# Kernel optimization log

Measured on AMD Instinct MI355X. Metric: run time of the kernel, lower is better.

The kernel has to match this reference:

```python
import jax, jax.numpy as jnp
import numpy as np

B, T, F = 256, 2048, 20
H_NODES = 256


def _heaviside(x):
    # smooth heaviside approx used throughout the original module
    return (jnp.tanh(10.0 * x) + 1.0) * 0.5


def _evap(wu, wl, wd, pet):
    h = _heaviside
    et1 = h(wu - pet) * pet + h(pet - wu) * wu
    rp = h(pet - et1) * (pet - et1)  # h(-(pet-et1))*0 term vanishes
    et22 = h(rp - wl) * wl + h(wl - rp) * rp
    et2 = h(rp) * et22
    et33 = h(rp - et2 - wd) * wd + h(wd - (rp - et2)) * (rp - et2)
    et3 = h(rp - et2) * et33
    return et1, et2, et3


def _runoff(wu, wl, wd, p, wum, wlm, wdm, b, c):
    wum = wum * 19.9 + 0.1
    wlm = wlm * 30.0 + 60.0
    wdm = wdm * 60.0 + 60.0
    c = c * 0.19 + 0.01
    b = b * 0.3 + 0.1
    w_total = wum + wlm + wdm
    s = c * (wu / w_total) ** 2 + b * (wl / w_total) ** 2
    return _heaviside(p - s) * (p - s)


def _partition(runoff, k1, k2, k3):
    k1 = k1 * 0.69 + 0.01
    k2 = k2 * 0.69 + 0.01
    k3 = k3 * 0.89 + 0.01
    sr = k1 * runoff
    itf = k2 * (runoff - sr)
    bf = k3 * (runoff - sr - itf)
    return sr, itf, bf


def setup_inputs() -> dict:
    key = jax.random.key(0)
    ks = jax.random.split(key, 7)
    u = lambda k, shp: jax.random.uniform(k, shp, jnp.float32, -0.05, 0.05)
    inputs = jax.random.uniform(ks[0], (B, T, F), jnp.float32)
    return {
        "inputs": inputs,
        "w1": u(ks[1], (15, H_NODES)),
        "b1": jnp.zeros((H_NODES,), jnp.float32),
        "w2": u(ks[2], (H_NODES, 64)),
        "b2": jnp.zeros((64,), jnp.float32),
        "w3": u(ks[3], (64, 8)),
        "b3": jnp.zeros((8,), jnp.float32),
    }


def reference(inputs, w1, b1, w2, b2, w3, b3):
    pet = inputs[..., 0:1]
    tmean = inputs[..., 1:2]
    p = inputs[..., 2:3]
    attrs = inputs[..., 5:]  # [B,T,15]

    # static-attribute -> physical-parameter MLP
    h1 = jnp.tanh(attrs @ w1 + b1)
    h2 = jnp.tanh(h1 @ w2 + b2)
    params = jax.nn.sigmoid(h2 @ w3 + b3)  # [B,T,8]

    xs = jnp.concatenate([pet, p, tmean, params], axis=-1)  # [B,T,11]

    def step(state, x):
        wu, wl, wd = state[:, 0:1], state[:, 1:2], state[:, 2:3]
        pet_t, p_t = x[:, 0:1], x[:, 1:2]
        et1, et2, et3 = _evap(wu, wl, wd, pet_t)
        clip = lambda d: jnp.clip(d, -1e5, 1e5)
        wu_n = wu + clip(p_t - et1)
        wl_n = wl + clip(p_t - et1 - et2)
        wd_n = wd + clip(p_t - et1 - et2 - et3)
        ns = jnp.concatenate([wu_n, wl_n, wd_n], axis=1)  # [B,3]
        return ns, ns

    init = jnp.zeros((inputs.shape[0], 3), inputs.dtype)
    _, outs = jax.lax.scan(step, init, jnp.swapaxes(xs, 0, 1))  # [T,B,3]
    outputs = jnp.swapaxes(outs, 0, 1)  # [B,T,3]

    wu, wl, wd = outputs[..., 0:1], outputs[..., 1:2], outputs[..., 2:3]
    wum, wlm, wdm = params[..., 0:1], params[..., 1:2], params[..., 2:3]
    b, c = params[..., 3:4], params[..., 4:5]
    k1, k2, k3 = params[..., 5:6], params[..., 6:7], params[..., 7:8]

    et1, et2, et3 = _evap(wu, wl, wd, pet)
    # NOTE: original call() swaps (wl,wd) and (wlm,wdm) here - kept faithful
    runoff = _runoff(wu, wd, wl, p, wum, wdm, wlm, b, c)
    sr, itf, bf = _partition(runoff, k1, k2, k3)
    total_q = sr + itf * 0.5 + bf * 0.25  # flow routing
    return total_q  # [B,T,1]
```

## Files before the change

kernel.cpp:

```cpp
#include <hip/hip_runtime.h>

#define B_ 256
#define T_ 2048
#define F_ 20
#define NT (B_*T_)
#define CH 16
#define NCH (T_/CH)

typedef __bf16 bf16x8 __attribute__((ext_vector_type(8)));
typedef float  f32x4  __attribute__((ext_vector_type(4)));

__device__ __forceinline__ float ex2(float x){ return __builtin_amdgcn_exp2f(x); }
__device__ __forceinline__ float rcpf_(float x){ return __builtin_amdgcn_rcpf(x); }

#define K10F 28.853900817779268f
#define INVK 0.034657359027997264f
#define K1F   2.8853900817779268f
#define LOG2E 1.4426950408889634f

__device__ __forceinline__ float hside(float x){ return 1.0f - rcpf_(ex2(K10F*x) + 1.0f); }
__device__ __forceinline__ float tanh_f(float z){ return 1.0f - 2.0f*rcpf_(ex2(K1F*z) + 1.0f); }
__device__ __forceinline__ float sigmoid_f(float z){ return rcpf_(1.0f + ex2(-LOG2E*z)); }


__global__ __launch_bounds__(512, 4) void fused_kernel(const float* __restrict__ in,
    const float* __restrict__ w1, const float* __restrict__ b1,
    const float* __restrict__ w2, const float* __restrict__ b2,
    const float* __restrict__ w3, const float* __restrict__ b3,
    float* __restrict__ ws){
  extern __shared__ char sm[];
  float* params2 = ws + 2*(size_t)NT;

  if (blockIdx.x < 8) {
    float2* wwT = (float2*)ws;
    float2* ppL = (float2*)sm;
    float2* dkb = (float2*)(sm + 8192);
    float2* rhb = (float2*)(sm + 24576);
    float2* qbb = (float2*)(sm + 32768);
    float*  wub = (float*)(sm + 40960);
    float*  wdb = (float*)(sm + 57344);

    int tid  = threadIdx.x;
    int wv   = tid >> 6;
    int l64  = tid & 63;
    bool act = l64 < 32;
    int lane = l64 & 31;
    int boff = blockIdx.x * 32;
    int bmy  = boff + lane;

    float Wu = 0.0f, WL = 0.0f, WD = 0.0f;

    if (wv == 4 && act){
    float2 v[CH];
      #pragma unroll
      for (int s = 0; s < CH; ++s){
        float4 r4 = *(const float4*)(in + ((size_t)bmy*T_ + s)*F_);
        v[s] = make_float2(r4.x, r4.z);
      }
      #pragma unroll
      for (int s = 0; s < CH; ++s)
        ppL[s*32 + lane] = make_float2(K10F*v[s].x, K10F*(v[s].y - v[s].x));
    }
    __syncthreads();

    for (int it = 0; it < NCH + 4; ++it){
      if (wv == 0){
        int c = it;
        if (c < NCH && act){
          int par = c & 1, pd = c & 3, pw = c & 7;
          float2 pe[CH];
          #pragma unroll
          for (int s = 0; s < CH; ++s) pe[s] = ppL[(par*CH + s)*32 + lane];
          #pragma unroll
          for (int s = 0; s < CH; ++s){
            float t1 = Wu - pe[s].x;
            float r  = rcpf_(ex2(t1) + 1.0f);
            float dK = -t1*r;
            float BASE = pe[s].y + dK;
            float Wn = Wu + BASE;
            dkb[(pd*CH + s)*32 + lane] = make_float2(dK, BASE);
            wub[(pw*CH + s)*32 + lane] = Wn;
            Wu = Wn;
          }
        }
      } else if (wv == 1){
        int c = it - 1;
        if (c >= 0 && c < NCH && act){
          int par = c & 1, pd = c & 3;
          float dk[CH];
          #pragma unroll
          for (int s = 0; s < CH; ++s) dk[s] = dkb[(pd*CH + s)*32 + lane].x;
          #pragma unroll
          for (int s = 0; s < CH; ++s){
            float r1  = rcpf_(ex2(dk[s]) + 1.0f);
            float RP  = fmaf(-dk[s], r1, dk[s]);
            float HRP = 1.0f - rcpf_(ex2(RP) + 1.0f);
            rhb[(par*CH + s)*32 + lane] = make_float2(RP, HRP);
          }
        }
      } else if (wv == 2){
        int c = it - 2;
        if (c >= 0 && c < NCH && act){
          int par = c & 1, pd = c & 3;
          float2 rh[CH]; float bs[CH];
          #pragma unroll
          for (int s = 0; s < CH; ++s) rh[s] = rhb[(par*CH + s)*32 + lane];
          #pragma unroll
          for (int s = 0; s < CH; ++s) bs[s] = dkb[(pd*CH + s)*32 + lane].y;
          #pragma unroll
          for (int s = 0; s < CH; ++s){
            float D2   = rh[s].x - WL;
            float r    = rcpf_(ex2(D2) + 1.0f);
            float et22 = fmaf(D2, r, WL);
            float WLB  = WL + bs[s];
            float Wn   = fmaf(-rh[s].y, et22, WLB);
            float ET2  = rh[s].y * et22;
            qbb[(par*CH + s)*32 + lane] = make_float2(rh[s].x - ET2, bs[s] - ET2);
            WL = Wn;
          }
        }
      } else if (wv == 3){
        int c = it - 3;
        if (c >= 0 && c < NCH && act){
          int par = c & 1;
          float2 qb[CH];
          #pragma unroll
          for (int s = 0; s < CH; ++s) qb[s] = qbb[(par*CH + s)*32 + lane];
          #pragma unroll
          for (int s = 0; s < CH; ++s){
            float hqv  = 1.0f - rcpf_(ex2(qb[s].x) + 1.0f);
            float D3   = qb[s].x - WD;
            float r    = rcpf_(ex2(D3) + 1.0f);
            float et33 = fmaf(D3, r, WD);
            float WDB  = WD + qb[s].y;
            float Wn   = fmaf(-hqv, et33, WDB);
            wdb[(par*CH + s)*32 + lane] = Wn;
            WD = Wn;
          }
        }
      } else if (wv == 4){
        int cn = it + 1;
        if (cn < NCH && act){
          float2 v[CH];
          #pragma unroll
          for (int s = 0; s < CH; ++s){
            float4 r4 = *(const float4*)(in + ((size_t)bmy*T_ + cn*CH + s)*F_);
            v[s] = make_float2(r4.x, r4.z);
          }
          int par = cn & 1;
          #pragma unroll
          for (int s = 0; s < CH; ++s)
            ppL[(par*CH + s)*32 + lane] = make_float2(K10F*v[s].x, K10F*(v[s].y - v[s].x));
        }
      } else if (wv == 5){
        int c = it - 4;
        if (c >= 0 && c < NCH && act){
          int pw = c & 7, par = c & 1;
          float wuv[CH], wdv[CH];
          #pragma unroll
          for (int s = 0; s < CH; ++s) wuv[s] = wub[(pw*CH + s)*32 + lane];
          #pragma unroll
          for (int s = 0; s < CH; ++s) wdv[s] = wdb[(par*CH + s)*32 + lane];
          float2* dst = &wwT[(size_t)bmy*T_ + c*CH];
          #pragma unroll
          for (int s = 0; s < CH; ++s)
            dst[s] = make_float2(wuv[s]*INVK, wdv[s]*INVK);
        }
      }
      __syncthreads();
    }
    return;
  }

  __bf16* w1f  = (__bf16*)sm;
  __bf16* w2f  = (__bf16*)(sm + 8192);
  float*  b1s  = (float*)(sm + 40960);
  float*  b2s  = (float*)(sm + 41984);
  float*  w3s  = (float*)(sm + 42240);
  float*  b3s  = (float*)(sm + 44288);
  __bf16* hbufA= (__bf16*)(sm + 44320);

  int tid = threadIdx.x;

  for (int s = tid; s < 16*32*8; s += 512) w1f[s] = (__bf16)0.0f;
  __syncthreads();
  for (int idx = tid; idx < 15*256; idx += 512){
    int k = idx >> 8, n = idx & 255;
    int ct = n >> 4;
    int l  = ((k>>3)*16) + (n & 15);
    int j  = k & 7;
    w1f[(ct*32 + l)*8 + j] = (__bf16)w1[idx];
  }
  for (int idx = tid; idx < 256*64; idx += 512){
    int k = idx >> 6, n = idx & 63;
    int kb = k >> 5;
    int lq = (k >> 3) & 3;
    int j  = k & 7;
    int ct = n >> 4;
    int l  = lq*16 + (n & 15);
    w2f[((kb*4 + ct)*64 + l)*8 + j] = (__bf16)w2[idx];
  }
  if (tid < 256) b1s[tid] = b1[tid];
  if (tid < 64)  b2s[tid] = b2[tid];
  if (tid < 512) w3s[tid] = w3[tid];
  if (tid < 8)   b3s[tid] = b3[tid];
  __syncthreads();

  int lane = tid & 63;
  int wv   = tid >> 6;
  int m    = lane & 15;
  int q    = lane >> 4;
  int r0   = (blockIdx.x - 8)*128 + wv*16;

  int rho = r0 + m;
  const float* ap = in + (size_t)rho*F_ + 5;
  bf16x8 a1;
  #pragma unroll
  for (int j = 0; j < 8; ++j){
    int k = q*8 + j;
    float v = (k < 15) ? ap[k] : 0.0f;
    a1[j] = (__bf16)v;
  }

  __bf16* hb = hbufA + wv*1152;
  f32x4 zero4 = {0.0f, 0.0f, 0.0f, 0.0f};
  bf16x8 zero8;
  #pragma unroll
  for (int j = 0; j < 8; ++j) zero8[j] = (__bf16)0.0f;

  f32x4 acc2[4] = {zero4, zero4, zero4, zero4};

  #pragma unroll
  for (int p = 0; p < 4; ++p){
    #pragma unroll
    for (int c4 = 0; c4 < 4; ++c4){
      int ct = p*4 + c4;
      bf16x8 bw = zero8;
      if (lane < 32) bw = *(const bf16x8*)&w1f[(ct*32 + lane)*8];
      f32x4 c1 = __builtin_amdgcn_mfma_f32_16x16x32_bf16(a1, bw, zero4, 0, 0, 0);
      int f = c4*16 + m;
      float bb = b1s[p*64 + f];
      #pragma unroll
      for (int i = 0; i < 4; ++i){
        float h = tanh_f(c1[i] + bb);
        hb[(q*4 + i)*72 + f] = (__bf16)h;
      }
    }
    #pragma unroll
    for (int kb = 0; kb < 2; ++kb){
      bf16x8 a2 = *(const bf16x8*)&hb[m*72 + q*8 + kb*32];
      #pragma unroll
      for (int ct = 0; ct < 4; ++ct){
        bf16x8 bw2 = *(const bf16x8*)&w2f[(((p*2 + kb)*4 + ct)*64 + lane)*8];
        acc2[ct] = __builtin_amdgcn_mfma_f32_16x16x32_bf16(a2, bw2, acc2[ct], 0, 0, 0);
      }
    }
  }

  #pragma unroll
  for (int ct = 0; ct < 4; ++ct){
    int f = ct*16 + m;
    float bb = b2s[f];
    #pragma unroll
    for (int i = 0; i < 4; ++i){
      float h = tanh_f(acc2[ct][i] + bb);
      hb[(q*4 + i)*72 + f] = (__bf16)h;
    }
  }

  float z0 = b3s[2*q], z1 = b3s[2*q + 1];
  #pragma unroll
  for (int kb3 = 0; kb3 < 8; ++kb3){
    bf16x8 hv8 = *(const bf16x8*)&hb[m*72 + kb3*8];
    #pragma unroll
    for (int j = 0; j < 8; ++j){
      float hv = (float)hv8[j];
      int k = kb3*8 + j;
      z0 = fmaf(hv, w3s[k*8 + 2*q],     z0);
      z1 = fmaf(hv, w3s[k*8 + 2*q + 1], z1);
    }
  }
  float2 outp = make_float2(sigmoid_f(z0), sigmoid_f(z1));
  *(float2*)&params2[(size_t)rho*8 + 2*q] = outp;
}

__global__ __launch_bounds__(256) void final_kernel(const float* __restrict__ in,
                                                    const float* __restrict__ ws,
                                                    float* __restrict__ out){
  int rho = blockIdx.x*256 + threadIdx.x;
  if (rho >= NT) return;
  const float2* wwT = (const float2*)ws;
  const float* params2 = ws + 2*(size_t)NT;

  float p  = in[(size_t)rho*F_ + 2];
  float2 w = wwT[rho];
  float wu = w.x, wd = w.y;
  const float4* pp = (const float4*)(params2 + (size_t)rho*8);
  float4 p0 = pp[0], p1 = pp[1];
  float wum   = fmaf(p0.x, 19.9f, 0.1f);
  float wlm_s = fmaf(p0.z, 30.0f, 60.0f);
  float wdm_s = fmaf(p0.y, 60.0f, 60.0f);
  float cc = fmaf(p1.x, 0.19f, 0.01f);
  float bcoef = fmaf(p0.w, 0.30f, 0.10f);
  float wt = wum + wlm_s + wdm_s;
  float xu = wu / wt;
  float xd = wd / wt;
  float s  = cc*xu*xu + bcoef*xd*xd;
  float ps = p - s;
  float runoff = hside(ps)*ps;
  float k1p = fmaf(p1.y, 0.69f, 0.01f);
  float k2p = fmaf(p1.z, 0.69f, 0.01f);
  float k3p = fmaf(p1.w, 0.89f, 0.01f);
  float sr  = k1p*runoff;
  float itf = k2p*(runoff - sr);
  float bf  = k3p*(runoff - sr - itf);
  out[rho] = sr + 0.5f*itf + 0.25f*bf;
}

extern "C" void kernel_launch(void* const* d_in, const int* in_sizes, int n_in,
                              void* d_out, int out_size, void* d_ws, size_t ws_size,
                              hipStream_t stream) {
  const float* in = (const float*)d_in[0];
  const float* w1 = (const float*)d_in[1];
  const float* b1 = (const float*)d_in[2];
  const float* w2 = (const float*)d_in[3];
  const float* b2 = (const float*)d_in[4];
  const float* w3 = (const float*)d_in[5];
  const float* b3 = (const float*)d_in[6];
  float* out = (float*)d_out;
  float* ws  = (float*)d_ws;

  fused_kernel<<<NT/128 + 8,  512, 62752, stream>>>(in, w1, b1, w2, b2, w3, b3, ws);
  final_kernel<<<NT/256,      256, 0,     stream>>>(in, ws, out);
}
```

Measured before the change: 245.0 us.

## Deepen scan wavefront pipeline to nine stages and stage precipitation for final kernel

Splits the serial scan pipeline into more warp-specialized stages, moving the heaviside computations for RP and qv off the recurrence-critical waves. Dedicated writer waves store wu and wd as separate contiguous float4 arrays. The loader wave double-buffers global input in registers and also writes a compact precipitation array, so the final kernel no longer does strided reads of the input. Blocks grow to 576 threads with static shared memory, which adds pipeline latency, raises register pressure and changes occupancy for the MLP blocks, where the extra wave idles.

```diff
diff --git a/kernel.cpp b/kernel.cpp
--- a/kernel.cpp
+++ b/kernel.cpp
@@ -23,148 +23,229 @@
 __device__ __forceinline__ float sigmoid_f(float z){ return rcpf_(1.0f + ex2(-LOG2E*z)); }
 
 
-__global__ __launch_bounds__(512, 4) void fused_kernel(const float* __restrict__ in,
+struct ScanS {
+  float2 ppL[2][CH][32];
+  float  dkR[2][CH][32];
+  float  bsR[4][CH][32];
+  float  wuR[2][CH][32];
+  float  rpR[4][CH][32];
+  float  hrR[2][CH][32];
+  float  qvR[4][CH][32];
+  float  b2R[4][CH][32];
+  float  hqR[2][CH][32];
+  float  wdR[2][CH][32];
+};
+struct MlpS {
+  __bf16 w1f[16*32*8];
+  __bf16 w2f[32*64*8];
+  float  b1s[256];
+  float  b2s[64];
+  float  w3s[512];
+  float  b3s[8];
+  __bf16 hbuf[8][1152];
+};
+union SMu { ScanS s; MlpS m; };
+
+__global__ __launch_bounds__(576) void fused_kernel(const float* __restrict__ in,
     const float* __restrict__ w1, const float* __restrict__ b1,
     const float* __restrict__ w2, const float* __restrict__ b2,
     const float* __restrict__ w3, const float* __restrict__ b3,
     float* __restrict__ ws){
-  extern __shared__ char sm[];
+  __shared__ SMu smu;
   float* params2 = ws + 2*(size_t)NT;
 
   if (blockIdx.x < 8) {
-    float2* wwT = (float2*)ws;
-    float2* ppL = (float2*)sm;
-    float2* dkb = (float2*)(sm + 8192);
-    float2* rhb = (float2*)(sm + 24576);
-    float2* qbb = (float2*)(sm + 32768);
-    float*  wub = (float*)(sm + 40960);
-    float*  wdb = (float*)(sm + 57344);
-
+    ScanS& S = smu.s;
+    float* wuT = ws;
+    float* wdT = ws + (size_t)NT;
+    float* pT  = ws + 10*(size_t)NT;
     int tid  = threadIdx.x;
     int wv   = tid >> 6;
-    int l64  = tid & 63;
-    bool act = l64 < 32;
-    int lane = l64 & 31;
-    int boff = blockIdx.x * 32;
-    int bmy  = boff + lane;
+    int lane = tid & 31;
+    bool act = (tid & 63) < 32;
+    int bmy  = blockIdx.x*32 + lane;
+    const float* inb = in + (size_t)bmy*T_*F_;
 
     float Wu = 0.0f, WL = 0.0f, WD = 0.0f;
-
-    if (wv == 4 && act){
     float2 v[CH];
+
+    if (wv == 6 && act){
       #pragma unroll
       for (int s = 0; s < CH; ++s){
-        float4 r4 = *(const float4*)(in + ((size_t)bmy*T_ + s)*F_);
+        float4 r4 = *(const float4*)(inb + (size_t)s*F_);
         v[s] = make_float2(r4.x, r4.z);
       }
       #pragma unroll
       for (int s = 0; s < CH; ++s)
-        ppL[s*32 + lane] = make_float2(K10F*v[s].x, K10F*(v[s].y - v[s].x));
+        S.ppL[0][s][lane] = make_float2(K10F*v[s].x, K10F*(v[s].y - v[s].x));
+      float* pdst = &pT[(size_t)bmy*T_];
+      #pragma unroll
+      for (int g = 0; g < 4; ++g)
+        *(float4*)(pdst + g*4) = make_float4(v[g*4].y, v[g*4+1].y, v[g*4+2].y, v[g*4+3].y);
+      #pragma unroll
+      for (int s = 0; s < CH; ++s){
+        float4 r4 = *(const float4*)(inb + (size_t)(CH + s)*F_);
+        v[s] = make_float2(r4.x, r4.z);
+      }
     }
     __syncthreads();
 
-    for (int it = 0; it < NCH + 4; ++it){
+    for (int it = 0; it < NCH + 6; ++it){
       if (wv == 0){
         int c = it;
         if (c < NCH && act){
-          int par = c & 1, pd = c & 3, pw = c & 7;
           float2 pe[CH];
           #pragma unroll
-          for (int s = 0; s < CH; ++s) pe[s] = ppL[(par*CH + s)*32 + lane];
+          for (int s = 0; s < CH; ++s) pe[s] = S.ppL[c&1][s][lane];
+          float dk_[CH], bs_[CH], wu_[CH];
           #pragma unroll
           for (int s = 0; s < CH; ++s){
             float t1 = Wu - pe[s].x;
             float r  = rcpf_(ex2(t1) + 1.0f);
             float dK = -t1*r;
-            float BASE = pe[s].y + dK;
-            float Wn = Wu + BASE;
-            dkb[(pd*CH + s)*32 + lane] = make_float2(dK, BASE);
-            wub[(pw*CH + s)*32 + lane] = Wn;
-            Wu = Wn;
+            float BS = pe[s].y + dK;
+            Wu += BS;
+            dk_[s] = dK; bs_[s] = BS; wu_[s] = Wu;
           }
+          #pragma unroll
+          for (int s = 0; s < CH; ++s) S.dkR[c&1][s][lane] = dk_[s];
+          #pragma unroll
+          for (int s = 0; s < CH; ++s) S.bsR[c&3][s][lane] = bs_[s];
+          #pragma unroll
+          for (int s = 0; s < CH; ++s) S.wuR[c&1][s][lane] = wu_[s];
         }
       } else if (wv == 1){
         int c = it - 1;
         if (c >= 0 && c < NCH && act){
-          int par = c & 1, pd = c & 3;
-          float dk[CH];
-          #pragma unroll
-          for (int s = 0; s < CH; ++s) dk[s] = dkb[(pd*CH + s)*32 + lane].x;
+          float dk_[CH];
+          #pragma unroll
+          for (int s = 0; s < CH; ++s) dk_[s] = S.dkR[c&1][s][lane];
+          float rp_[CH];
           #pragma unroll
           for (int s = 0; s < CH; ++s){
-            float r1  = rcpf_(ex2(dk[s]) + 1.0f);
-            float RP  = fmaf(-dk[s], r1, dk[s]);
-            float HRP = 1.0f - rcpf_(ex2(RP) + 1.0f);
-            rhb[(par*CH + s)*32 + lane] = make_float2(RP, HRP);
+            float r1 = rcpf_(ex2(dk_[s]) + 1.0f);
+            rp_[s] = fmaf(-dk_[s], r1, dk_[s]);
           }
+          #pragma unroll
+          for (int s = 0; s < CH; ++s) S.rpR[c&3][s][lane] = rp_[s];
         }
       } else if (wv == 2){
         int c = it - 2;
         if (c >= 0 && c < NCH && act){
-          int par = c & 1, pd = c & 3;
-          float2 rh[CH]; float bs[CH];
-          #pragma unroll
-          for (int s = 0; s < CH; ++s) rh[s] = rhb[(par*CH + s)*32 + lane];
-          #pragma unroll
-          for (int s = 0; s < CH; ++s) bs[s] = dkb[(pd*CH + s)*32 + lane].y;
+          float rp_[CH];
+          #pragma unroll
+          for (int s = 0; s < CH; ++s) rp_[s] = S.rpR[c&3][s][lane];
+          float hr_[CH];
+          #pragma unroll
+          for (int s = 0; s < CH; ++s) hr_[s] = 1.0f - rcpf_(ex2(rp_[s]) + 1.0f);
+          #pragma unroll
+          for (int s = 0; s < CH; ++s) S.hrR[c&1][s][lane] = hr_[s];
+        }
+      } else if (wv == 3){
+        int c = it - 3;
+        if (c >= 0 && c < NCH && act){
+          float rp_[CH], hr_[CH], bs_[CH];
+          #pragma unroll
+          for (int s = 0; s < CH; ++s) rp_[s] = S.rpR[c&3][s][lane];
+          #pragma unroll
+          for (int s = 0; s < CH; ++s) hr_[s] = S.hrR[c&1][s][lane];
+          #pragma unroll
+          for (int s = 0; s < CH; ++s) bs_[s] = S.bsR[c&3][s][lane];
+          float qv_[CH], b2_[CH];
           #pragma unroll
           for (int s = 0; s < CH; ++s){
-            float D2   = rh[s].x - WL;
+            float D2   = rp_[s] - WL;
             float r    = rcpf_(ex2(D2) + 1.0f);
             float et22 = fmaf(D2, r, WL);
-            float WLB  = WL + bs[s];
-            float Wn   = fmaf(-rh[s].y, et22, WLB);
-            float ET2  = rh[s].y * et22;
-            qbb[(par*CH + s)*32 + lane] = make_float2(rh[s].x - ET2, bs[s] - ET2);
-            WL = Wn;
+            float WLB  = WL + bs_[s];
+            float ET2  = hr_[s]*et22;
+            WL = fmaf(-hr_[s], et22, WLB);
+            qv_[s] = rp_[s] - ET2;
+            b2_[s] = bs_[s] - ET2;
           }
-        }
-      } else if (wv == 3){
-        int c = it - 3;
-        if (c >= 0 && c < NCH && act){
-          int par = c & 1;
-          float2 qb[CH];
-          #pragma unroll
-          for (int s = 0; s < CH; ++s) qb[s] = qbb[(par*CH + s)*32 + lane];
+          #pragma unroll
+          for (int s = 0; s < CH; ++s) S.qvR[c&3][s][lane] = qv_[s];
+          #pragma unroll
+          for (int s = 0; s < CH; ++s) S.b2R[c&3][s][lane] = b2_[s];
+        }
+      } else if (wv == 4){
+        int c = it - 4;
+        if (c >= 0 && c < NCH && act){
+          float qv_[CH];
+          #pragma unroll
+          for (int s = 0; s < CH; ++s) qv_[s] = S.qvR[c&3][s][lane];
+          float hq_[CH];
+          #pragma unroll
+          for (int s = 0; s < CH; ++s) hq_[s] = 1.0f - rcpf_(ex2(qv_[s]) + 1.0f);
+          #pragma unroll
+          for (int s = 0; s < CH; ++s) S.hqR[c&1][s][lane] = hq_[s];
+        }
+      } else if (wv == 5){
+        int c = it - 5;
+        if (c >= 0 && c < NCH && act){
+          float qv_[CH], hq_[CH], b2_[CH];
+          #pragma unroll
+          for (int s = 0; s < CH; ++s) qv_[s] = S.qvR[c&3][s][lane];
+          #pragma unroll
+          for (int s = 0; s < CH; ++s) hq_[s] = S.hqR[c&1][s][lane];
+          #pragma unroll
+          for (int s = 0; s < CH; ++s) b2_[s] = S.b2R[c&3][s][lane];
+          float wd_[CH];
           #pragma unroll
           for (int s = 0; s < CH; ++s){
-            float hqv  = 1.0f - rcpf_(ex2(qb[s].x) + 1.0f);
-            float D3   = qb[s].x - WD;
+            float D3   = qv_[s] - WD;
             float r    = rcpf_(ex2(D3) + 1.0f);
             float et33 = fmaf(D3, r, WD);
-            float WDB  = WD + qb[s].y;
-            float Wn   = fmaf(-hqv, et33, WDB);
-            wdb[(par*CH + s)*32 + lane] = Wn;
-            WD = Wn;
+            float WDB  = WD + b2_[s];
+            WD = fmaf(-hq_[s], et33, WDB);
+            wd_[s] = WD;
           }
-        }
-      } else if (wv == 4){
-        int cn = it + 1;
-        if (cn < NCH && act){
-          float2 v[CH];
-          #pragma unroll
-          for (int s = 0; s < CH; ++s){
-            float4 r4 = *(const float4*)(in + ((size_t)bmy*T_ + cn*CH + s)*F_);
-            v[s] = make_float2(r4.x, r4.z);
+          #pragma unroll
+          for (int s = 0; s < CH; ++s) S.wdR[c&1][s][lane] = wd_[s];
+        }
+      } else if (wv == 6){
+        int n = it + 1;
+        if (n < NCH && act){
+          float2 w[CH];
+          #pragma unroll
+          for (int s = 0; s < CH; ++s) w[s] = v[s];
+          #pragma unroll
+          for (int s = 0; s < CH; ++s)
+            S.ppL[n&1][s][lane] = make_float2(K10F*w[s].x, K10F*(w[s].y - w[s].x));
+          float* pdst = &pT[(size_t)bmy*T_ + n*CH];
+          #pragma unroll
+          for (int g = 0; g < 4; ++g)
+            *(float4*)(pdst + g*4) = make_float4(w[g*4].y, w[g*4+1].y, w[g*4+2].y, w[g*4+3].y);
+          int n2 = it + 2;
+          if (n2 < NCH){
+            #pragma unroll
+            for (int s = 0; s < CH; ++s){
+              float4 r4 = *(const float4*)(inb + (size_t)(n2*CH + s)*F_);
+              v[s] = make_float2(r4.x, r4.z);
+            }
           }
-          int par = cn & 1;
-          #pragma unroll
-          for (int s = 0; s < CH; ++s)
-            ppL[(par*CH + s)*32 + lane] = make_float2(K10F*v[s].x, K10F*(v[s].y - v[s].x));
-        }
-      } else if (wv == 5){
-        int c = it - 4;
-        if (c >= 0 && c < NCH && act){
-          int pw = c & 7, par = c & 1;
-          float wuv[CH], wdv[CH];
-          #pragma unroll
-          for (int s = 0; s < CH; ++s) wuv[s] = wub[(pw*CH + s)*32 + lane];
-          #pragma unroll
-          for (int s = 0; s < CH; ++s) wdv[s] = wdb[(par*CH + s)*32 + lane];
-          float2* dst = &wwT[(size_t)bmy*T_ + c*CH];
-          #pragma unroll
-          for (int s = 0; s < CH; ++s)
-            dst[s] = make_float2(wuv[s]*INVK, wdv[s]*INVK);
+        }
+      } else if (wv == 7){
+        int c = it - 1;
+        if (c >= 0 && c < NCH && act){
+          float wu_[CH];
+          #pragma unroll
+          for (int s = 0; s < CH; ++s) wu_[s] = S.wuR[c&1][s][lane] * INVK;
+          float* dst = &wuT[(size_t)bmy*T_ + c*CH];
+          #pragma unroll
+          for (int g = 0; g < 4; ++g)
+            *(float4*)(dst + g*4) = make_float4(wu_[g*4], wu_[g*4+1], wu_[g*4+2], wu_[g*4+3]);
+        }
+      } else {
+        int c = it - 6;
+        if (c >= 0 && c < NCH && act){
+          float wd_[CH];
+          #pragma unroll
+          for (int s = 0; s < CH; ++s) wd_[s] = S.wdR[c&1][s][lane] * INVK;
+          float* dst = &wdT[(size_t)bmy*T_ + c*CH];
+          #pragma unroll
+          for (int g = 0; g < 4; ++g)
+            *(float4*)(dst + g*4) = make_float4(wd_[g*4], wd_[g*4+1], wd_[g*4+2], wd_[g*4+3]);
         }
       }
       __syncthreads();
@@ -172,42 +253,36 @@
     return;
   }
 
-  __bf16* w1f  = (__bf16*)sm;
-  __bf16* w2f  = (__bf16*)(sm + 8192);
-  float*  b1s  = (float*)(sm + 40960);
-  float*  b2s  = (float*)(sm + 41984);
-  float*  w3s  = (float*)(sm + 42240);
-  float*  b3s  = (float*)(sm + 44288);
-  __bf16* hbufA= (__bf16*)(sm + 44320);
-
+  MlpS& M = smu.m;
   int tid = threadIdx.x;
 
-  for (int s = tid; s < 16*32*8; s += 512) w1f[s] = (__bf16)0.0f;
+  for (int s = tid; s < 16*32*8; s += 576) M.w1f[s] = (__bf16)0.0f;
   __syncthreads();
-  for (int idx = tid; idx < 15*256; idx += 512){
+  for (int idx = tid; idx < 15*256; idx += 576){
     int k = idx >> 8, n = idx & 255;
     int ct = n >> 4;
     int l  = ((k>>3)*16) + (n & 15);
     int j  = k & 7;
-    w1f[(ct*32 + l)*8 + j] = (__bf16)w1[idx];
-  }
-  for (int idx = tid; idx < 256*64; idx += 512){
+    M.w1f[(ct*32 + l)*8 + j] = (__bf16)w1[idx];
+  }
+  for (int idx = tid; idx < 256*64; idx += 576){
     int k = idx >> 6, n = idx & 63;
     int kb = k >> 5;
     int lq = (k >> 3) & 3;
     int j  = k & 7;
     int ct = n >> 4;
     int l  = lq*16 + (n & 15);
-    w2f[((kb*4 + ct)*64 + l)*8 + j] = (__bf16)w2[idx];
-  }
-  if (tid < 256) b1s[tid] = b1[tid];
-  if (tid < 64)  b2s[tid] = b2[tid];
-  if (tid < 512) w3s[tid] = w3[tid];
-  if (tid < 8)   b3s[tid] = b3[tid];
+    M.w2f[((kb*4 + ct)*64 + l)*8 + j] = (__bf16)w2[idx];
+  }
+  if (tid < 256) M.b1s[tid] = b1[tid];
+  if (tid < 64)  M.b2s[tid] = b2[tid];
+  if (tid < 512) M.w3s[tid] = w3[tid];
+  if (tid < 8)   M.b3s[tid] = b3[tid];
   __syncthreads();
 
+  int wv = tid >> 6;
+  if (wv >= 8) return;
   int lane = tid & 63;
-  int wv   = tid >> 6;
   int m    = lane & 15;
   int q    = lane >> 4;
   int r0   = (blockIdx.x - 8)*128 + wv*16;
@@ -218,11 +293,11 @@
   #pragma unroll
   for (int j = 0; j < 8; ++j){
     int k = q*8 + j;
-    float v = (k < 15) ? ap[k] : 0.0f;
-    a1[j] = (__bf16)v;
-  }
-
-  __bf16* hb = hbufA + wv*1152;
+    float vv = (k < 15) ? ap[k] : 0.0f;
+    a1[j] = (__bf16)vv;
+  }
+
+  __bf16* hb = M.hbuf[wv];
   f32x4 zero4 = {0.0f, 0.0f, 0.0f, 0.0f};
   bf16x8 zero8;
   #pragma unroll
@@ -236,10 +311,10 @@
     for (int c4 = 0; c4 < 4; ++c4){
       int ct = p*4 + c4;
       bf16x8 bw = zero8;
-      if (lane < 32) bw = *(const bf16x8*)&w1f[(ct*32 + lane)*8];
+      if (lane < 32) bw = *(const bf16x8*)&M.w1f[(ct*32 + lane)*8];
       f32x4 c1 = __builtin_amdgcn_mfma_f32_16x16x32_bf16(a1, bw, zero4, 0, 0, 0);
       int f = c4*16 + m;
-      float bb = b1s[p*64 + f];
+      float bb = M.b1s[p*64 + f];
       #pragma unroll
       for (int i = 0; i < 4; ++i){
         float h = tanh_f(c1[i] + bb);
@@ -251,7 +326,7 @@
       bf16x8 a2 = *(const bf16x8*)&hb[m*72 + q*8 + kb*32];
       #pragma unroll
       for (int ct = 0; ct < 4; ++ct){
-        bf16x8 bw2 = *(const bf16x8*)&w2f[(((p*2 + kb)*4 + ct)*64 + lane)*8];
+        bf16x8 bw2 = *(const bf16x8*)&M.w2f[(((p*2 + kb)*4 + ct)*64 + lane)*8];
         acc2[ct] = __builtin_amdgcn_mfma_f32_16x16x32_bf16(a2, bw2, acc2[ct], 0, 0, 0);
       }
     }
@@ -260,7 +335,7 @@
   #pragma unroll
   for (int ct = 0; ct < 4; ++ct){
     int f = ct*16 + m;
-    float bb = b2s[f];
+    float bb = M.b2s[f];
     #pragma unroll
     for (int i = 0; i < 4; ++i){
       float h = tanh_f(acc2[ct][i] + bb);
@@ -268,7 +343,7 @@
     }
   }
 
-  float z0 = b3s[2*q], z1 = b3s[2*q + 1];
+  float z0 = M.b3s[2*q], z1 = M.b3s[2*q + 1];
   #pragma unroll
   for (int kb3 = 0; kb3 < 8; ++kb3){
     bf16x8 hv8 = *(const bf16x8*)&hb[m*72 + kb3*8];
@@ -276,25 +351,25 @@
     for (int j = 0; j < 8; ++j){
       float hv = (float)hv8[j];
       int k = kb3*8 + j;
-      z0 = fmaf(hv, w3s[k*8 + 2*q],     z0);
-      z1 = fmaf(hv, w3s[k*8 + 2*q + 1], z1);
+      z0 = fmaf(hv, M.w3s[k*8 + 2*q],     z0);
+      z1 = fmaf(hv, M.w3s[k*8 + 2*q + 1], z1);
     }
   }
   float2 outp = make_float2(sigmoid_f(z0), sigmoid_f(z1));
   *(float2*)&params2[(size_t)rho*8 + 2*q] = outp;
 }
 
-__global__ __launch_bounds__(256) void final_kernel(const float* __restrict__ in,
-                                                    const float* __restrict__ ws,
+__global__ __launch_bounds__(256) void final_kernel(const float* __restrict__ ws,
                                                     float* __restrict__ out){
   int rho = blockIdx.x*256 + threadIdx.x;
   if (rho >= NT) return;
-  const float2* wwT = (const float2*)ws;
+  const float* wuT = ws;
+  const float* wdT = ws + (size_t)NT;
   const float* params2 = ws + 2*(size_t)NT;
-
-  float p  = in[(size_t)rho*F_ + 2];
-  float2 w = wwT[rho];
-  float wu = w.x, wd = w.y;
+  const float* pT  = ws + 10*(size_t)NT;
+
+  float p  = pT[rho];
+  float wu = wuT[rho], wd = wdT[rho];
   const float4* pp = (const float4*)(params2 + (size_t)rho*8);
   float4 p0 = pp[0], p1 = pp[1];
   float wum   = fmaf(p0.x, 19.9f, 0.1f);
@@ -330,6 +405,6 @@
   float* out = (float*)d_out;
   float* ws  = (float*)d_ws;
 
-  fused_kernel<<<NT/128 + 8,  512, 62752, stream>>>(in, w1, b1, w2, b2, w3, b3, ws);
-  final_kernel<<<NT/256,      256, 0,     stream>>>(in, ws, out);
+  fused_kernel<<<NT/128 + 8, 576, 0, stream>>>(in, w1, b1, w2, b2, w3, b3, ws);
+  final_kernel<<<NT/256,     256, 0, stream>>>(ws, out);
 }
```

Result: slower. 313.1 us (+27.8%).
